# Kernel optimization log

Measured on AMD Instinct MI355X. Metric: run time of the kernel, lower is better.

Reference implementation:

```python
import jax, jax.numpy as jnp
import numpy as np

V_TH = 1.0  # spikingjelly IFNode default threshold; v starts at 0, hard reset after fire


def setup_inputs() -> dict:
    key = jax.random.key(0)
    k_x, k_w1, k_w2 = jax.random.split(key, 3)
    B, IN, FEAT, OUT = 4096, 3136, 6272, 500
    # binary input spikes (LatencyEncoder emits 0/1 spikes per timestep)
    x = (jax.random.uniform(k_x, (B, IN)) < 0.5).astype(jnp.float32)
    # Linear weights, torch layout [out_features, in_features], kaiming-ish scale
    W1 = jax.random.normal(k_w1, (FEAT, IN), dtype=jnp.float32) / np.sqrt(IN)
    W2 = jax.random.normal(k_w2, (OUT, FEAT), dtype=jnp.float32) / np.sqrt(FEAT)
    return {"x": x, "W1": W1, "W2": W2}


def reference(x, W1, W2):
    # Linear (no bias) -> IF neuron single step: v = 0 + I; spike = (v >= V_TH); hard reset
    v1 = x @ W1.T                      # [B, FEAT]
    s1 = (v1 >= V_TH).astype(x.dtype)  # binary hidden spikes
    v2 = s1 @ W2.T                     # [B, OUT]
    s2 = (v2 >= V_TH).astype(x.dtype)  # output spikes
    return s2
```

## Files before the change

kernel.cpp:

```cpp
#include <hip/hip_runtime.h>


namespace {
constexpr int kB = 4096;
constexpr int kIn = 3136;
constexpr int kFeat = 6272;
constexpr int kFeatWords = 196;
constexpr int kOut = 500;
constexpr size_t kPlane1 = (size_t)kFeat * kIn;
constexpr size_t kW1F = 3 * kPlane1;
constexpr size_t kW2F = (size_t)784 * 12288;
constexpr size_t kS1Bytes = (size_t)kB * kFeatWords * 4;
constexpr size_t kXb2Bytes = (size_t)49 * kB * 8;
constexpr unsigned kCap1 = 2u << 20;
constexpr unsigned kCap2 = 1u << 16;
__device__ constexpr double kTau1 = 7.4769e-4;
__device__ constexpr double kTau2 = 1.4955e-3;
}

typedef int v4i __attribute__((ext_vector_type(4)));
typedef int v16i __attribute__((ext_vector_type(16)));

__device__ __forceinline__ void gload_lds16(const void* g, void* l) {
  __builtin_amdgcn_global_load_lds((__attribute__((address_space(1))) void*)(g),
                                   (__attribute__((address_space(3))) void*)(l),
                                   16, 0, 0);
}

__device__ __forceinline__ v4i expand16(unsigned b) {
  unsigned u0 = (((b      ) & 0xFu) * 0x204081u) & 0x01010101u;
  unsigned u1 = (((b >> 4 ) & 0xFu) * 0x204081u) & 0x01010101u;
  unsigned u2 = (((b >> 8 ) & 0xFu) * 0x204081u) & 0x01010101u;
  unsigned u3 = (((b >> 12) & 0xFu) * 0x204081u) & 0x01010101u;
  return (v4i){(int)u0, (int)u1, (int)u2, (int)u3};
}

__device__ __forceinline__ void split3(float w, signed char* d) {
  float c = rintf(w * 128.f);
  d[0] = (signed char)(int)c;
  float r = fmaf(c, -7.8125e-03f, w);
  c = rintf(r * 16384.f);
  d[1] = (signed char)(int)c;
  r = fmaf(c, -6.103515625e-05f, r);
  c = rintf(r * 2097152.f);
  d[2] = (signed char)(int)c;
}

__global__ __launch_bounds__(256) void conv_w1F(const float* __restrict__ W,
                                                signed char* __restrict__ F) {
  const int bx = blockIdx.x;
  const int fb = bx / 49;
  const int kt = bx % 49;
  const int f = threadIdx.x & 63;
  const int g = threadIdx.x >> 6;
  const float* src = W + (size_t)(fb * 64 + f) * kIn + kt * 64 + g * 16;
  union { signed char c[16]; int4 v; } o[3];
#pragma unroll
  for (int q = 0; q < 4; ++q) {
    const float4 w = *(const float4*)(src + q * 4);
    signed char d[4][3];
    split3(w.x, d[0]); split3(w.y, d[1]); split3(w.z, d[2]); split3(w.w, d[3]);
#pragma unroll
    for (int e = 0; e < 4; ++e)
#pragma unroll
      for (int j = 0; j < 3; ++j) o[j].c[q * 4 + e] = d[e][j];
  }
#pragma unroll
  for (int j = 0; j < 3; ++j)
    *(int4*)(F + ((size_t)bx * 3 + j) * 4096 + g * 1024 + f * 16) = o[j].v;
}

__global__ __launch_bounds__(256) void conv_w2F(const float* __restrict__ W,
                                                signed char* __restrict__ F) {
  const int bx = blockIdx.x;
  const int fb = bx / 98;
  const int kt = bx % 98;
  const int f = threadIdx.x & 63;
  const int g = threadIdx.x >> 6;
  const int feat = fb * 64 + f;
  union { signed char c[16]; int4 v; } o[3];
#pragma unroll
  for (int q = 0; q < 4; ++q) {
    float4 w = {0.f, 0.f, 0.f, 0.f};
    if (feat < kOut)
      w = *(const float4*)(W + (size_t)feat * kFeat + kt * 64 + g * 16 + q * 4);
    signed char d[4][3];
    split3(w.x, d[0]); split3(w.y, d[1]); split3(w.z, d[2]); split3(w.w, d[3]);
#pragma unroll
    for (int e = 0; e < 4; ++e)
#pragma unroll
      for (int j = 0; j < 3; ++j) o[j].c[q * 4 + e] = d[e][j];
  }
#pragma unroll
  for (int j = 0; j < 3; ++j)
    *(int4*)(F + ((size_t)bx * 3 + j) * 4096 + g * 1024 + f * 16) = o[j].v;
}

__global__ __launch_bounds__(256) void pack_x2(const float* __restrict__ X,
                                               uint2* __restrict__ xb2) {
  const int wid = (blockIdx.x * 256 + threadIdx.x) >> 6;
  const int lane = threadIdx.x & 63;
  const int b = wid / 49;
  const int g = wid % 49;
  const float v = X[(size_t)b * kIn + g * 64 + lane];
  const unsigned long long bal = __ballot(v != 0.f);
  if (lane == 0) xb2[(size_t)g * kB + b] = make_uint2((unsigned)bal, (unsigned)(bal >> 32));
}

__global__ __launch_bounds__(512, 4) void fc1_v10(
    const uint2* __restrict__ xb2, const signed char* __restrict__ w1lF,
    unsigned* __restrict__ s1b, unsigned* __restrict__ s1T,
    unsigned* __restrict__ cnt, unsigned* __restrict__ list) {
  __shared__ __align__(16) signed char lds[24576];
  const int tid = threadIdx.x;
  const int lane = tid & 63;
  const int ln31 = lane & 31;
  const int half = lane >> 5;
  const int wv = tid >> 6;
  const int waveM = wv >> 1;
  const int waveN = wv & 1;

  const int lin = blockIdx.x + 16 * blockIdx.y;
  const int sw = (lin & 7) * 196 + (lin >> 3);
  const int bx = sw >> 4;
  const int bM = (sw & 15) * 256;

  const signed char* const gbase = w1lF + (size_t)bx * 49 * 12288;
  const bool has1 = (wv < 4);
  const unsigned sG0 = wv * 1024u + lane * 16u;
  const unsigned sL0 = wv * 1024u;
  const unsigned sG1 = (wv + 8) * 1024u + lane * 16u;
  const unsigned sL1 = (wv + 8) * 1024u;

  const uint2* const aptr = xb2 + bM + waveM * 64 + ln31;
  const unsigned bfeat = (waveN * 32 + ln31) * 16u;

  v16i acc[2][3] = {};
  uint2 aC0, aC1, aN0, aN1;

  gload_lds16(gbase + sG0, lds + sL0);
  if (has1) gload_lds16(gbase + sG1, lds + sL1);
  aC0 = aptr[0];
  aC1 = aptr[32];
  const uint2* apn = aptr + (size_t)kB;
  const signed char* gstage = gbase + 12288;

  for (int kt = 0; kt < 49; ++kt) {
    __syncthreads();
    const int cb = (kt & 1) * 12288;
    if (kt < 48) {
      const int nb = ((kt + 1) & 1) * 12288;
      gload_lds16(gstage + sG0, lds + nb + sL0);
      if (has1) gload_lds16(gstage + sG1, lds + nb + sL1);
      gstage += 12288;
      aN0 = apn[0];
      aN1 = apn[32];
      apn += (size_t)kB;
    }
#pragma unroll
    for (int kk = 0; kk < 2; ++kk) {
      const unsigned gsel = (kk * 2 + half) * 1024u;
      const v4i b0 = *(const v4i*)(lds + cb + 0 * 4096 + gsel + bfeat);
      const v4i b1 = *(const v4i*)(lds + cb + 1 * 4096 + gsel + bfeat);
      const v4i b2 = *(const v4i*)(lds + cb + 2 * 4096 + gsel + bfeat);
      const unsigned w0 = kk ? aC0.y : aC0.x;
      const v4i a0 = expand16((w0 >> (half * 16)) & 0xFFFFu);
      acc[0][0] = __builtin_amdgcn_mfma_i32_32x32x32_i8(a0, b0, acc[0][0], 0, 0, 0);
      acc[0][1] = __builtin_amdgcn_mfma_i32_32x32x32_i8(a0, b1, acc[0][1], 0, 0, 0);
      acc[0][2] = __builtin_amdgcn_mfma_i32_32x32x32_i8(a0, b2, acc[0][2], 0, 0, 0);
      const unsigned w1 = kk ? aC1.y : aC1.x;
      const v4i a1 = expand16((w1 >> (half * 16)) & 0xFFFFu);
      acc[1][0] = __builtin_amdgcn_mfma_i32_32x32x32_i8(a1, b0, acc[1][0], 0, 0, 0);
      acc[1][1] = __builtin_amdgcn_mfma_i32_32x32x32_i8(a1, b1, acc[1][1], 0, 0, 0);
      acc[1][2] = __builtin_amdgcn_mfma_i32_32x32x32_i8(a1, b2, acc[1][2], 0, 0, 0);
    }
    aC0 = aN0;
    aC1 = aN1;
  }

  const double s7 = 0.0078125;
  const int word = bx * 2 + waveN;
  const int fcol = word * 32 + ln31;
#pragma unroll
  for (int sub = 0; sub < 2; ++sub) {
#pragma unroll
    for (int t = 0; t < 16; ++t) {
      double v = (double)acc[sub][2][t];
      v = v * s7 + (double)acc[sub][1][t];
      v = v * s7 + (double)acc[sub][0][t];
      v = v * s7;
      const unsigned long long bal = __ballot(v >= 1.0);
      const int mrow = bM + waveM * 64 + sub * 32 + (t & 3) + 8 * (t >> 2);
      if (lane == 0) {
        s1b[(size_t)mrow * kFeatWords + word] = (unsigned)bal;
        s1T[(size_t)word * kB + mrow] = (unsigned)bal;
      }
      if (lane == 32) {
        s1b[(size_t)(mrow + 4) * kFeatWords + word] = (unsigned)(bal >> 32);
        s1T[(size_t)word * kB + mrow + 4] = (unsigned)(bal >> 32);
      }
      if (fabs(v - 1.0) <= kTau1) {
        const unsigned idx = atomicAdd(cnt, 1u);
        if (idx < kCap1) list[idx] = ((unsigned)(mrow + 4 * half) << 13) | (unsigned)fcol;
      }
    }
  }
}

__global__ __launch_bounds__(256) void fc1_correct(
    const float* __restrict__ x, const float* __restrict__ W1,
    const unsigned* __restrict__ cnt, const unsigned* __restrict__ list,
    unsigned* __restrict__ s1b, unsigned* __restrict__ s1T) {
  const unsigned n = min(cnt[0], kCap1);
  const int lane = threadIdx.x & 63;
  const int wid = (blockIdx.x * 256 + threadIdx.x) >> 6;
  const int nw = (gridDim.x * 256) >> 6;
  for (unsigned i = wid; i < n; i += nw) {
    const unsigned u = list[i];
    const int b = (int)(u >> 13);
    const int f = (int)(u & 8191u);
    double s = 0.0;
    for (int k = lane; k < kIn; k += 64)
      s = fma((double)x[(size_t)b * kIn + k], (double)W1[(size_t)f * kIn + k], s);
#pragma unroll
    for (int off = 32; off > 0; off >>= 1) s += __shfl_down(s, off);
    if (lane == 0) {
      const unsigned mask = 1u << (f & 31);
      unsigned* p1 = s1b + (size_t)b * kFeatWords + (f >> 5);
      unsigned* p2 = s1T + (size_t)(f >> 5) * kB + b;
      if (s >= 1.0) { atomicOr(p1, mask); atomicOr(p2, mask); }
      else          { atomicAnd(p1, ~mask); atomicAnd(p2, ~mask); }
    }
  }
}

__global__ __launch_bounds__(128, 4) void fc2_v7(
    const unsigned* __restrict__ s1T, const signed char* __restrict__ w2lF,
    float* __restrict__ out, unsigned* __restrict__ cnt,
    unsigned* __restrict__ list) {
  const int tid = threadIdx.x;
  const int lane = tid & 63;
  const int ln31 = lane & 31;
  const int half = lane >> 5;
  const int wvN = tid >> 6;

  const int lin = blockIdx.x + 128 * blockIdx.y;
  const int sw = ((lin & 7) << 7) + (lin >> 3);
  const int bx = sw >> 7;
  const int bM = (sw & 127) * 32;

  const unsigned* const aptr = s1T + bM + ln31;
  const int fl = wvN * 32 + ln31;
  const signed char* const bbase =
      w2lF + (size_t)(bx * 98) * 12288 + half * 1024u + fl * 16u;

  v16i acc[3] = {};
  v4i b0[6], b1[6];
  uint2 a0, a1;

#define LOAD_TILE(nk, bf, ab)                                   \
  {                                                             \
    const signed char* bp = bbase + (size_t)(nk) * 12288;       \
    bf[0] = *(const v4i*)(bp);                                  \
    bf[1] = *(const v4i*)(bp + 2048);                           \
    bf[2] = *(const v4i*)(bp + 4096);                           \
    bf[3] = *(const v4i*)(bp + 6144);                           \
    bf[4] = *(const v4i*)(bp + 8192);                           \
    bf[5] = *(const v4i*)(bp + 10240);                          \
    (ab).x = aptr[(size_t)((nk) * 2) * kB];                     \
    (ab).y = aptr[(size_t)((nk) * 2 + 1) * kB];                 \
  }
#define COMPUTE_TILE(bf, ab)                                                    \
  {                                                                             \
    _Pragma("unroll")                                                           \
    for (int kk = 0; kk < 2; ++kk) {                                            \
      const unsigned word = kk ? (ab).y : (ab).x;                               \
      const v4i a = expand16((word >> (half * 16)) & 0xFFFFu);                  \
      acc[0] = __builtin_amdgcn_mfma_i32_32x32x32_i8(a, bf[kk], acc[0], 0,0,0); \
      acc[1] = __builtin_amdgcn_mfma_i32_32x32x32_i8(a, bf[2+kk], acc[1],0,0,0);\
      acc[2] = __builtin_amdgcn_mfma_i32_32x32x32_i8(a, bf[4+kk], acc[2],0,0,0);\
    }                                                                           \
  }

  LOAD_TILE(0, b0, a0);
  for (int kt = 0; kt + 2 <= 98; kt += 2) {
    LOAD_TILE(kt + 1, b1, a1);
    COMPUTE_TILE(b0, a0);
    const int nk2 = (kt + 2 < 98) ? kt + 2 : 97;
    LOAD_TILE(nk2, b0, a0);
    COMPUTE_TILE(b1, a1);
  }

  const double s7 = 0.0078125;
  const int o = bx * 64 + wvN * 32 + ln31;
#pragma unroll
  for (int t = 0; t < 16; ++t) {
    double v = (double)acc[2][t];
    v = v * s7 + (double)acc[1][t];
    v = v * s7 + (double)acc[0][t];
    v = v * s7;
    const int b = bM + (t & 3) + 8 * (t >> 2) + 4 * half;
    if (o < kOut) {
      out[(size_t)b * kOut + o] = (v >= 1.0) ? 1.0f : 0.0f;
      if (fabs(v - 1.0) <= kTau2) {
        const unsigned idx = atomicAdd(cnt, 1u);
        if (idx < kCap2) list[idx] = ((unsigned)b << 13) | (unsigned)o;
      }
    }
  }
#undef LOAD_TILE
#undef COMPUTE_TILE
}

__global__ __launch_bounds__(256) void fc2_correct(
    const unsigned* __restrict__ s1b, const float* __restrict__ W2,
    const unsigned* __restrict__ cnt, const unsigned* __restrict__ list,
    float* __restrict__ out) {
  const unsigned n = min(cnt[0], kCap2);
  const int lane = threadIdx.x & 63;
  const int wid = (blockIdx.x * 256 + threadIdx.x) >> 6;
  const int nw = (gridDim.x * 256) >> 6;
  for (unsigned i = wid; i < n; i += nw) {
    const unsigned u = list[i];
    const int b = (int)(u >> 13);
    const int o = (int)(u & 8191u);
    double s = 0.0;
    for (int k = lane; k < kFeat; k += 64) {
      const unsigned w = s1b[(size_t)b * kFeatWords + (k >> 5)];
      if ((w >> (k & 31)) & 1u) s += (double)W2[(size_t)o * kFeat + k];
    }
#pragma unroll
    for (int off = 32; off > 0; off >>= 1) s += __shfl_down(s, off);
    if (lane == 0) out[(size_t)b * kOut + o] = (s >= 1.0) ? 1.0f : 0.0f;
  }
}

__global__ __launch_bounds__(256) void snn_fc1(const float* __restrict__ x,
                                               const float* __restrict__ W1,
                                               unsigned int* __restrict__ s1bits) {
  __shared__ double Xd[32][66];
  __shared__ double Wd[32][66];
  __shared__ unsigned int spikes[64][2];
  const int tid = threadIdx.x;
  const int tx = tid & 15;
  const int ty = tid >> 4;
  const int b0 = blockIdx.y * 64;
  const int f0 = blockIdx.x * 64;
  if (tid < 128) spikes[tid >> 1][tid & 1] = 0u;
  double acc[4][4];
#pragma unroll
  for (int j = 0; j < 4; ++j)
#pragma unroll
    for (int i = 0; i < 4; ++i) acc[j][i] = 0.0;
  const int rl = tid >> 2;
  const int kq = (tid & 3) * 8;
  const float* xrow = x + (size_t)(b0 + rl) * kIn + kq;
  const float* wrow = W1 + (size_t)(f0 + rl) * kIn + kq;
  for (int kc = 0; kc < kIn; kc += 32) {
    const float4 xv0 = *(const float4*)(xrow + kc);
    const float4 xv1 = *(const float4*)(xrow + kc + 4);
    const float4 wv0 = *(const float4*)(wrow + kc);
    const float4 wv1 = *(const float4*)(wrow + kc + 4);
    __syncthreads();
    Xd[kq + 0][rl] = (double)xv0.x; Xd[kq + 1][rl] = (double)xv0.y;
    Xd[kq + 2][rl] = (double)xv0.z; Xd[kq + 3][rl] = (double)xv0.w;
    Xd[kq + 4][rl] = (double)xv1.x; Xd[kq + 5][rl] = (double)xv1.y;
    Xd[kq + 6][rl] = (double)xv1.z; Xd[kq + 7][rl] = (double)xv1.w;
    Wd[kq + 0][rl] = (double)wv0.x; Wd[kq + 1][rl] = (double)wv0.y;
    Wd[kq + 2][rl] = (double)wv0.z; Wd[kq + 3][rl] = (double)wv0.w;
    Wd[kq + 4][rl] = (double)wv1.x; Wd[kq + 5][rl] = (double)wv1.y;
    Wd[kq + 6][rl] = (double)wv1.z; Wd[kq + 7][rl] = (double)wv1.w;
    __syncthreads();
#pragma unroll
    for (int k = 0; k < 32; ++k) {
      const double2 xa = *(const double2*)&Xd[k][ty * 4];
      const double2 xb = *(const double2*)&Xd[k][ty * 4 + 2];
      const double2 wa = *(const double2*)&Wd[k][tx * 4];
      const double2 wb = *(const double2*)&Wd[k][tx * 4 + 2];
      const double xv[4] = {xa.x, xa.y, xb.x, xb.y};
      const double wv[4] = {wa.x, wa.y, wb.x, wb.y};
#pragma unroll
      for (int j = 0; j < 4; ++j)
#pragma unroll
        for (int i = 0; i < 4; ++i) acc[j][i] += xv[j] * wv[i];
    }
  }
  __syncthreads();
#pragma unroll
  for (int j = 0; j < 4; ++j) {
    unsigned int nib = 0u;
#pragma unroll
    for (int i = 0; i < 4; ++i) nib |= (acc[j][i] >= 1.0 ? 1u : 0u) << i;
    atomicOr(&spikes[ty * 4 + j][tx >> 3], nib << ((tx * 4) & 31));
  }
  __syncthreads();
  if (tid < 128) {
    const int r = tid >> 1;
    const int w = tid & 1;
    s1bits[(size_t)(b0 + r) * kFeatWords + (f0 >> 5) + w] = spikes[r][w];
  }
}

__global__ __launch_bounds__(256) void snn_fc2(const unsigned int* __restrict__ s1bits,
                                               const float* __restrict__ W2,
                                               float* __restrict__ out) {
  __shared__ double Wd[32][66];
  __shared__ unsigned int Sb[64];
  const int tid = threadIdx.x;
  const int tx = tid & 15;
  const int ty = tid >> 4;
  const int b0 = blockIdx.y * 64;
  const int o0 = blockIdx.x * 64;
  double acc[4][4];
#pragma unroll
  for (int j = 0; j < 4; ++j)
#pragma unroll
    for (int i = 0; i < 4; ++i) acc[j][i] = 0.0;
  const int rl = tid >> 2;
  const int kq = (tid & 3) * 8;
  int orow = o0 + rl;
  if (orow >= kOut) orow = kOut - 1;
  const float* wrow = W2 + (size_t)orow * kFeat + kq;
  for (int kc = 0; kc < kFeat; kc += 32) {
    const float4 wv0 = *(const float4*)(wrow + kc);
    const float4 wv1 = *(const float4*)(wrow + kc + 4);
    unsigned int sword = 0u;
    if (tid < 64) sword = s1bits[(size_t)(b0 + tid) * kFeatWords + (kc >> 5)];
    __syncthreads();
    Wd[kq + 0][rl] = (double)wv0.x; Wd[kq + 1][rl] = (double)wv0.y;
    Wd[kq + 2][rl] = (double)wv0.z; Wd[kq + 3][rl] = (double)wv0.w;
    Wd[kq + 4][rl] = (double)wv1.x; Wd[kq + 5][rl] = (double)wv1.y;
    Wd[kq + 6][rl] = (double)wv1.z; Wd[kq + 7][rl] = (double)wv1.w;
    if (tid < 64) Sb[tid] = sword;
    __syncthreads();
    const unsigned int rw0 = Sb[ty * 4 + 0];
    const unsigned int rw1 = Sb[ty * 4 + 1];
    const unsigned int rw2 = Sb[ty * 4 + 2];
    const unsigned int rw3 = Sb[ty * 4 + 3];
#pragma unroll
    for (int k = 0; k < 32; ++k) {
      const double2 wa = *(const double2*)&Wd[k][tx * 4];
      const double2 wb = *(const double2*)&Wd[k][tx * 4 + 2];
      const double wv[4] = {wa.x, wa.y, wb.x, wb.y};
      const double sv[4] = {(double)((rw0 >> k) & 1u), (double)((rw1 >> k) & 1u),
                            (double)((rw2 >> k) & 1u), (double)((rw3 >> k) & 1u)};
#pragma unroll
      for (int j = 0; j < 4; ++j)
#pragma unroll
        for (int i = 0; i < 4; ++i) acc[j][i] += sv[j] * wv[i];
    }
  }
#pragma unroll
  for (int j = 0; j < 4; ++j) {
    const int b = b0 + ty * 4 + j;
#pragma unroll
    for (int i = 0; i < 4; ++i) {
      const int o = o0 + tx * 4 + i;
      if (o < kOut) out[(size_t)b * kOut + o] = (acc[j][i] >= 1.0) ? 1.0f : 0.0f;
    }
  }
}

extern "C" void kernel_launch(void* const* d_in, const int* in_sizes, int n_in,
                              void* d_out, int out_size, void* d_ws, size_t ws_size,
                              hipStream_t stream) {
  const float* x = (const float*)d_in[0];
  const float* W1 = (const float*)d_in[1];
  const float* W2 = (const float*)d_in[2];
  float* out = (float*)d_out;

  char* p = (char*)d_ws;
  signed char* w1lF = (signed char*)p;   p += kW1F;
  signed char* w2lF = (signed char*)p;   p += kW2F;
  unsigned* s1b = (unsigned*)p;          p += kS1Bytes;
  unsigned* s1T = (unsigned*)p;          p += kS1Bytes;
  uint2* xb2 = (uint2*)p;                p += kXb2Bytes;
  unsigned* list1 = (unsigned*)p;        p += (size_t)kCap1 * 4;
  unsigned* list2 = (unsigned*)p;        p += (size_t)kCap2 * 4;
  unsigned* ctrs = (unsigned*)p;         p += 256;
  const size_t need = (size_t)(p - (char*)d_ws);

  if (ws_size >= need) {
    hipMemsetAsync(ctrs, 0, 32, stream);
    conv_w1F<<<4802, 256, 0, stream>>>(W1, w1lF);
    conv_w2F<<<784, 256, 0, stream>>>(W2, w2lF);
    pack_x2<<<50176, 256, 0, stream>>>(x, xb2);
    fc1_v10<<<dim3(16, 98), 512, 0, stream>>>(xb2, w1lF, s1b, s1T, ctrs, list1);
    fc1_correct<<<1024, 256, 0, stream>>>(x, W1, ctrs, list1, s1b, s1T);
    fc2_v7<<<dim3(128, 8), 128, 0, stream>>>(s1T, w2lF, out, ctrs + 4, list2);
    fc2_correct<<<64, 256, 0, stream>>>(s1b, W2, ctrs + 4, list2, out);
  } else {
    unsigned* s1 = (unsigned*)d_ws;
    snn_fc1<<<dim3(98, 64), 256, 0, stream>>>(x, W1, s1);
    snn_fc2<<<dim3(8, 64), 256, 0, stream>>>(s1, W2, out);
  }
}
```

Before: 576.3 us.

## Pre-expand input spikes to int8 MFMA-ready layout instead of bitpacked words

Replaces the bit-packed input format with an int8 layout pre-tiled to match the MFMA A-operand fragment order. The fc1 kernel can then load A fragments directly with 16-byte loads instead of expanding bits in registers each iteration. The pack kernel becomes fewer, wider blocks doing coalesced float4 reads. In exchange, fc1 reads 8x more A-operand bytes from global memory and more registers are live; launch bounds drop to 2 blocks per SM and the correction-list capacity is halved.

```diff
diff --git a/kernel.cpp b/kernel.cpp
--- a/kernel.cpp
+++ b/kernel.cpp
@@ -11,8 +11,8 @@
 constexpr size_t kW1F = 3 * kPlane1;
 constexpr size_t kW2F = (size_t)784 * 12288;
 constexpr size_t kS1Bytes = (size_t)kB * kFeatWords * 4;
-constexpr size_t kXb2Bytes = (size_t)49 * kB * 8;
-constexpr unsigned kCap1 = 2u << 20;
+constexpr size_t kX8Bytes = (size_t)49 * 256 * 1024;
+constexpr unsigned kCap1 = 1u << 20;
 constexpr unsigned kCap2 = 1u << 16;
 __device__ constexpr double kTau1 = 7.4769e-4;
 __device__ constexpr double kTau2 = 1.4955e-3;
@@ -96,19 +96,30 @@
     *(int4*)(F + ((size_t)bx * 3 + j) * 4096 + g * 1024 + f * 16) = o[j].v;
 }
 
-__global__ __launch_bounds__(256) void pack_x2(const float* __restrict__ X,
-                                               uint2* __restrict__ xb2) {
-  const int wid = (blockIdx.x * 256 + threadIdx.x) >> 6;
+__global__ __launch_bounds__(256) void pack_x8(const float* __restrict__ X,
+                                               signed char* __restrict__ xb8) {
+  const int slot = blockIdx.x * 4 + (threadIdx.x >> 6);
   const int lane = threadIdx.x & 63;
-  const int b = wid / 49;
-  const int g = wid % 49;
-  const float v = X[(size_t)b * kIn + g * 64 + lane];
-  const unsigned long long bal = __ballot(v != 0.f);
-  if (lane == 0) xb2[(size_t)g * kB + b] = make_uint2((unsigned)bal, (unsigned)(bal >> 32));
-}
-
-__global__ __launch_bounds__(512, 4) void fc1_v10(
-    const uint2* __restrict__ xb2, const signed char* __restrict__ w1lF,
+  const int kk = slot & 1;
+  const int mgrp = (slot >> 1) & 127;
+  const int kt = slot >> 8;
+  const int row = mgrp * 32 + (lane & 31);
+  const int k0 = kt * 64 + kk * 32 + (lane >> 5) * 16;
+  const float* src = X + (size_t)row * kIn + k0;
+  union { signed char c[16]; int4 v; } o;
+#pragma unroll
+  for (int q = 0; q < 4; ++q) {
+    const float4 w = *(const float4*)(src + q * 4);
+    o.c[q * 4 + 0] = (w.x != 0.f) ? 1 : 0;
+    o.c[q * 4 + 1] = (w.y != 0.f) ? 1 : 0;
+    o.c[q * 4 + 2] = (w.z != 0.f) ? 1 : 0;
+    o.c[q * 4 + 3] = (w.w != 0.f) ? 1 : 0;
+  }
+  *(int4*)(xb8 + (size_t)slot * 1024 + lane * 16) = o.v;
+}
+
+__global__ __launch_bounds__(512, 2) void fc1_v11(
+    const signed char* __restrict__ xb8, const signed char* __restrict__ w1lF,
     unsigned* __restrict__ s1b, unsigned* __restrict__ s1T,
     unsigned* __restrict__ cnt, unsigned* __restrict__ list) {
   __shared__ __align__(16) signed char lds[24576];
@@ -132,17 +143,22 @@
   const unsigned sG1 = (wv + 8) * 1024u + lane * 16u;
   const unsigned sL1 = (wv + 8) * 1024u;
 
-  const uint2* const aptr = xb2 + bM + waveM * 64 + ln31;
+  const int gmgrp0 = (bM >> 5) + waveM * 2;
+  const signed char* apn =
+      xb8 + ((size_t)gmgrp0 * 2) * 1024 + lane * 16u;
   const unsigned bfeat = (waveN * 32 + ln31) * 16u;
 
   v16i acc[2][3] = {};
-  uint2 aC0, aC1, aN0, aN1;
+  v4i c00, c01, c10, c11;
+  v4i n00, n01, n10, n11;
 
   gload_lds16(gbase + sG0, lds + sL0);
   if (has1) gload_lds16(gbase + sG1, lds + sL1);
-  aC0 = aptr[0];
-  aC1 = aptr[32];
-  const uint2* apn = aptr + (size_t)kB;
+  c00 = *(const v4i*)(apn);
+  c01 = *(const v4i*)(apn + 1024);
+  c10 = *(const v4i*)(apn + 2048);
+  c11 = *(const v4i*)(apn + 3072);
+  apn += 262144;
   const signed char* gstage = gbase + 12288;
 
   for (int kt = 0; kt < 49; ++kt) {
@@ -153,29 +169,37 @@
       gload_lds16(gstage + sG0, lds + nb + sL0);
       if (has1) gload_lds16(gstage + sG1, lds + nb + sL1);
       gstage += 12288;
-      aN0 = apn[0];
-      aN1 = apn[32];
-      apn += (size_t)kB;
-    }
-#pragma unroll
-    for (int kk = 0; kk < 2; ++kk) {
-      const unsigned gsel = (kk * 2 + half) * 1024u;
+      n00 = *(const v4i*)(apn);
+      n01 = *(const v4i*)(apn + 1024);
+      n10 = *(const v4i*)(apn + 2048);
+      n11 = *(const v4i*)(apn + 3072);
+      apn += 262144;
+    }
+    {
+      const unsigned gsel = half * 1024u;
       const v4i b0 = *(const v4i*)(lds + cb + 0 * 4096 + gsel + bfeat);
       const v4i b1 = *(const v4i*)(lds + cb + 1 * 4096 + gsel + bfeat);
       const v4i b2 = *(const v4i*)(lds + cb + 2 * 4096 + gsel + bfeat);
-      const unsigned w0 = kk ? aC0.y : aC0.x;
-      const v4i a0 = expand16((w0 >> (half * 16)) & 0xFFFFu);
-      acc[0][0] = __builtin_amdgcn_mfma_i32_32x32x32_i8(a0, b0, acc[0][0], 0, 0, 0);
-      acc[0][1] = __builtin_amdgcn_mfma_i32_32x32x32_i8(a0, b1, acc[0][1], 0, 0, 0);
-      acc[0][2] = __builtin_amdgcn_mfma_i32_32x32x32_i8(a0, b2, acc[0][2], 0, 0, 0);
-      const unsigned w1 = kk ? aC1.y : aC1.x;
-      const v4i a1 = expand16((w1 >> (half * 16)) & 0xFFFFu);
-      acc[1][0] = __builtin_amdgcn_mfma_i32_32x32x32_i8(a1, b0, acc[1][0], 0, 0, 0);
-      acc[1][1] = __builtin_amdgcn_mfma_i32_32x32x32_i8(a1, b1, acc[1][1], 0, 0, 0);
-      acc[1][2] = __builtin_amdgcn_mfma_i32_32x32x32_i8(a1, b2, acc[1][2], 0, 0, 0);
-    }
-    aC0 = aN0;
-    aC1 = aN1;
+      acc[0][0] = __builtin_amdgcn_mfma_i32_32x32x32_i8(c00, b0, acc[0][0], 0, 0, 0);
+      acc[0][1] = __builtin_amdgcn_mfma_i32_32x32x32_i8(c00, b1, acc[0][1], 0, 0, 0);
+      acc[0][2] = __builtin_amdgcn_mfma_i32_32x32x32_i8(c00, b2, acc[0][2], 0, 0, 0);
+      acc[1][0] = __builtin_amdgcn_mfma_i32_32x32x32_i8(c10, b0, acc[1][0], 0, 0, 0);
+      acc[1][1] = __builtin_amdgcn_mfma_i32_32x32x32_i8(c10, b1, acc[1][1], 0, 0, 0);
+      acc[1][2] = __builtin_amdgcn_mfma_i32_32x32x32_i8(c10, b2, acc[1][2], 0, 0, 0);
+    }
+    {
+      const unsigned gsel = (2 + half) * 1024u;
+      const v4i b0 = *(const v4i*)(lds + cb + 0 * 4096 + gsel + bfeat);
+      const v4i b1 = *(const v4i*)(lds + cb + 1 * 4096 + gsel + bfeat);
+      const v4i b2 = *(const v4i*)(lds + cb + 2 * 4096 + gsel + bfeat);
+      acc[0][0] = __builtin_amdgcn_mfma_i32_32x32x32_i8(c01, b0, acc[0][0], 0, 0, 0);
+      acc[0][1] = __builtin_amdgcn_mfma_i32_32x32x32_i8(c01, b1, acc[0][1], 0, 0, 0);
+      acc[0][2] = __builtin_amdgcn_mfma_i32_32x32x32_i8(c01, b2, acc[0][2], 0, 0, 0);
+      acc[1][0] = __builtin_amdgcn_mfma_i32_32x32x32_i8(c11, b0, acc[1][0], 0, 0, 0);
+      acc[1][1] = __builtin_amdgcn_mfma_i32_32x32x32_i8(c11, b1, acc[1][1], 0, 0, 0);
+      acc[1][2] = __builtin_amdgcn_mfma_i32_32x32x32_i8(c11, b2, acc[1][2], 0, 0, 0);
+    }
+    c00 = n00; c01 = n01; c10 = n10; c11 = n11;
   }
 
   const double s7 = 0.0078125;
@@ -474,7 +498,7 @@
   signed char* w2lF = (signed char*)p;   p += kW2F;
   unsigned* s1b = (unsigned*)p;          p += kS1Bytes;
   unsigned* s1T = (unsigned*)p;          p += kS1Bytes;
-  uint2* xb2 = (uint2*)p;                p += kXb2Bytes;
+  signed char* xb8 = (signed char*)p;    p += kX8Bytes;
   unsigned* list1 = (unsigned*)p;        p += (size_t)kCap1 * 4;
   unsigned* list2 = (unsigned*)p;        p += (size_t)kCap2 * 4;
   unsigned* ctrs = (unsigned*)p;         p += 256;
@@ -484,8 +508,8 @@
     hipMemsetAsync(ctrs, 0, 32, stream);
     conv_w1F<<<4802, 256, 0, stream>>>(W1, w1lF);
     conv_w2F<<<784, 256, 0, stream>>>(W2, w2lF);
-    pack_x2<<<50176, 256, 0, stream>>>(x, xb2);
-    fc1_v10<<<dim3(16, 98), 512, 0, stream>>>(xb2, w1lF, s1b, s1T, ctrs, list1);
+    pack_x8<<<3136, 256, 0, stream>>>(x, xb8);
+    fc1_v11<<<dim3(16, 98), 512, 0, stream>>>(xb8, w1lF, s1b, s1T, ctrs, list1);
     fc1_correct<<<1024, 256, 0, stream>>>(x, W1, ctrs, list1, s1b, s1T);
     fc2_v7<<<dim3(128, 8), 128, 0, stream>>>(s1T, w2lF, out, ctrs + 4, list2);
     fc2_correct<<<64, 256, 0, stream>>>(s1b, W2, ctrs + 4, list2, out);
```

Measured after the change: 681.1 us. +18.2%, slower.

## Triple-buffer fc1 LDS pipeline with split-phase barriers and MFMA priority

Applied to the files above, without the earlier changes.

Replaces the double-buffered fc1 main loop with a three-stage LDS ring (prefetch two tiles ahead), split into two half-K phases, each with explicit vmcnt/lgkmcnt waits, barriers, sched_barrier and s_setprio around the MFMA block. The aim is to hide global-to-LDS load latency and keep the matrix cores busy. In exchange, LDS use per block grows, the occupancy hint drops from 4 to 2, and each tile now has more barriers. The list1 capacity is also halved.

```diff
diff --git a/kernel.cpp b/kernel.cpp
--- a/kernel.cpp
+++ b/kernel.cpp
@@ -12,7 +12,7 @@
 constexpr size_t kW2F = (size_t)784 * 12288;
 constexpr size_t kS1Bytes = (size_t)kB * kFeatWords * 4;
 constexpr size_t kXb2Bytes = (size_t)49 * kB * 8;
-constexpr unsigned kCap1 = 2u << 20;
+constexpr unsigned kCap1 = 1u << 20;
 constexpr unsigned kCap2 = 1u << 16;
 __device__ constexpr double kTau1 = 7.4769e-4;
 __device__ constexpr double kTau2 = 1.4955e-3;
@@ -107,11 +107,11 @@
   if (lane == 0) xb2[(size_t)g * kB + b] = make_uint2((unsigned)bal, (unsigned)(bal >> 32));
 }
 
-__global__ __launch_bounds__(512, 4) void fc1_v10(
+__global__ __launch_bounds__(512, 2) void fc1_v12(
     const uint2* __restrict__ xb2, const signed char* __restrict__ w1lF,
     unsigned* __restrict__ s1b, unsigned* __restrict__ s1T,
     unsigned* __restrict__ cnt, unsigned* __restrict__ list) {
-  __shared__ __align__(16) signed char lds[24576];
+  __shared__ __align__(16) signed char lds[36864];
   const int tid = threadIdx.x;
   const int lane = tid & 63;
   const int ln31 = lane & 31;
@@ -137,46 +137,89 @@
 
   v16i acc[2][3] = {};
   uint2 aC0, aC1, aN0, aN1;
-
+  v4i a00, a10, a01, a11;
+
+  aC0 = aptr[0];
+  aC1 = aptr[32];
   gload_lds16(gbase + sG0, lds + sL0);
   if (has1) gload_lds16(gbase + sG1, lds + sL1);
-  aC0 = aptr[0];
-  aC1 = aptr[32];
+  gload_lds16(gbase + 12288 + sG0, lds + 12288 + sL0);
+  if (has1) gload_lds16(gbase + 12288 + sG1, lds + 12288 + sL1);
+  if (has1) asm volatile("s_waitcnt vmcnt(2)" ::: "memory");
+  else      asm volatile("s_waitcnt vmcnt(1)" ::: "memory");
+  __builtin_amdgcn_s_barrier();
+  asm volatile("" ::: "memory");
+
   const uint2* apn = aptr + (size_t)kB;
-  const signed char* gstage = gbase + 12288;
-
-  for (int kt = 0; kt < 49; ++kt) {
-    __syncthreads();
-    const int cb = (kt & 1) * 12288;
-    if (kt < 48) {
-      const int nb = ((kt + 1) & 1) * 12288;
-      gload_lds16(gstage + sG0, lds + nb + sL0);
-      if (has1) gload_lds16(gstage + sG1, lds + nb + sL1);
-      gstage += 12288;
-      aN0 = apn[0];
-      aN1 = apn[32];
-      apn += (size_t)kB;
-    }
-#pragma unroll
-    for (int kk = 0; kk < 2; ++kk) {
-      const unsigned gsel = (kk * 2 + half) * 1024u;
-      const v4i b0 = *(const v4i*)(lds + cb + 0 * 4096 + gsel + bfeat);
-      const v4i b1 = *(const v4i*)(lds + cb + 1 * 4096 + gsel + bfeat);
-      const v4i b2 = *(const v4i*)(lds + cb + 2 * 4096 + gsel + bfeat);
-      const unsigned w0 = kk ? aC0.y : aC0.x;
-      const v4i a0 = expand16((w0 >> (half * 16)) & 0xFFFFu);
-      acc[0][0] = __builtin_amdgcn_mfma_i32_32x32x32_i8(a0, b0, acc[0][0], 0, 0, 0);
-      acc[0][1] = __builtin_amdgcn_mfma_i32_32x32x32_i8(a0, b1, acc[0][1], 0, 0, 0);
-      acc[0][2] = __builtin_amdgcn_mfma_i32_32x32x32_i8(a0, b2, acc[0][2], 0, 0, 0);
-      const unsigned w1 = kk ? aC1.y : aC1.x;
-      const v4i a1 = expand16((w1 >> (half * 16)) & 0xFFFFu);
-      acc[1][0] = __builtin_amdgcn_mfma_i32_32x32x32_i8(a1, b0, acc[1][0], 0, 0, 0);
-      acc[1][1] = __builtin_amdgcn_mfma_i32_32x32x32_i8(a1, b1, acc[1][1], 0, 0, 0);
-      acc[1][2] = __builtin_amdgcn_mfma_i32_32x32x32_i8(a1, b2, acc[1][2], 0, 0, 0);
-    }
-    aC0 = aN0;
-    aC1 = aN1;
-  }
+  const signed char* gst = gbase + 2 * 12288;
+
+#define FC1_MM(AS0, AS1, B0, B1, B2)                                          \
+  acc[0][0] = __builtin_amdgcn_mfma_i32_32x32x32_i8(AS0, B0, acc[0][0],0,0,0);\
+  acc[0][1] = __builtin_amdgcn_mfma_i32_32x32x32_i8(AS0, B1, acc[0][1],0,0,0);\
+  acc[0][2] = __builtin_amdgcn_mfma_i32_32x32x32_i8(AS0, B2, acc[0][2],0,0,0);\
+  acc[1][0] = __builtin_amdgcn_mfma_i32_32x32x32_i8(AS1, B0, acc[1][0],0,0,0);\
+  acc[1][1] = __builtin_amdgcn_mfma_i32_32x32x32_i8(AS1, B1, acc[1][1],0,0,0);\
+  acc[1][2] = __builtin_amdgcn_mfma_i32_32x32x32_i8(AS1, B2, acc[1][2],0,0,0)
+
+#define FC1_PH0(CB, SB, DO_A, DO_S)                                           \
+  {                                                                           \
+    a00 = expand16((aC0.x >> (half * 16)) & 0xFFFFu);                         \
+    a10 = expand16((aC1.x >> (half * 16)) & 0xFFFFu);                         \
+    a01 = expand16((aC0.y >> (half * 16)) & 0xFFFFu);                         \
+    a11 = expand16((aC1.y >> (half * 16)) & 0xFFFFu);                         \
+    const v4i b0 = *(const v4i*)(lds + (CB) + 0 * 4096 + half * 1024u + bfeat);\
+    const v4i b1 = *(const v4i*)(lds + (CB) + 1 * 4096 + half * 1024u + bfeat);\
+    const v4i b2 = *(const v4i*)(lds + (CB) + 2 * 4096 + half * 1024u + bfeat);\
+    if (DO_A) { aN0 = apn[0]; aN1 = apn[32]; apn += (size_t)kB; }             \
+    if (DO_S) { gload_lds16(gst + sG0, lds + (SB) + sL0); }                   \
+    asm volatile("" ::: "memory");                                            \
+    __builtin_amdgcn_s_barrier();                                             \
+    asm volatile("s_waitcnt lgkmcnt(0)" ::: "memory");                        \
+    __builtin_amdgcn_sched_barrier(0);                                        \
+    __builtin_amdgcn_s_setprio(1);                                            \
+    FC1_MM(a00, a10, b0, b1, b2);                                             \
+    __builtin_amdgcn_s_setprio(0);                                            \
+    __builtin_amdgcn_s_barrier();                                             \
+    asm volatile("" ::: "memory");                                            \
+  }
+
+#define FC1_PH1(CB, SB, DO_S, WAITM)                                          \
+  {                                                                           \
+    const v4i b0 = *(const v4i*)(lds + (CB) + 0 * 4096 + (2 + half) * 1024u + bfeat);\
+    const v4i b1 = *(const v4i*)(lds + (CB) + 1 * 4096 + (2 + half) * 1024u + bfeat);\
+    const v4i b2 = *(const v4i*)(lds + (CB) + 2 * 4096 + (2 + half) * 1024u + bfeat);\
+    if ((DO_S) && has1) { gload_lds16(gst + sG1, lds + (SB) + sL1); }         \
+    if ((DO_S)) gst += 12288;                                                 \
+    if ((WAITM) == 2) {                                                       \
+      if (has1) asm volatile("s_waitcnt vmcnt(2)" ::: "memory");              \
+      else      asm volatile("s_waitcnt vmcnt(1)" ::: "memory");              \
+    } else if ((WAITM) == 0) {                                                \
+      asm volatile("s_waitcnt vmcnt(0)" ::: "memory");                        \
+    }                                                                         \
+    asm volatile("" ::: "memory");                                            \
+    __builtin_amdgcn_s_barrier();                                             \
+    asm volatile("s_waitcnt lgkmcnt(0)" ::: "memory");                        \
+    __builtin_amdgcn_sched_barrier(0);                                        \
+    __builtin_amdgcn_s_setprio(1);                                            \
+    FC1_MM(a01, a11, b0, b1, b2);                                             \
+    __builtin_amdgcn_s_setprio(0);                                            \
+    __builtin_amdgcn_s_barrier();                                             \
+    asm volatile("" ::: "memory");                                            \
+    aC0 = aN0; aC1 = aN1;                                                     \
+  }
+
+  for (int t = 0; t < 15; ++t) {
+    FC1_PH0(0,     24576, 1, 1); FC1_PH1(0,     24576, 1, 2);
+    FC1_PH0(12288, 0,     1, 1); FC1_PH1(12288, 0,     1, 2);
+    FC1_PH0(24576, 12288, 1, 1); FC1_PH1(24576, 12288, 1, 2);
+  }
+  FC1_PH0(0,     24576, 1, 1); FC1_PH1(0,     24576, 1, 2);
+  FC1_PH0(12288, 0,     1, 1); FC1_PH1(12288, 0,     1, 2);
+  FC1_PH0(24576, 0,     1, 0); FC1_PH1(24576, 0,     0, 0);
+  FC1_PH0(0,     0,     0, 0); FC1_PH1(0,     0,     0, -1);
+#undef FC1_PH0
+#undef FC1_PH1
+#undef FC1_MM
 
   const double s7 = 0.0078125;
   const int word = bx * 2 + waveN;
@@ -485,7 +528,7 @@
     conv_w1F<<<4802, 256, 0, stream>>>(W1, w1lF);
     conv_w2F<<<784, 256, 0, stream>>>(W2, w2lF);
     pack_x2<<<50176, 256, 0, stream>>>(x, xb2);
-    fc1_v10<<<dim3(16, 98), 512, 0, stream>>>(xb2, w1lF, s1b, s1T, ctrs, list1);
+    fc1_v12<<<dim3(16, 98), 512, 0, stream>>>(xb2, w1lF, s1b, s1T, ctrs, list1);
     fc1_correct<<<1024, 256, 0, stream>>>(x, W1, ctrs, list1, s1b, s1T);
     fc2_v7<<<dim3(128, 8), 128, 0, stream>>>(s1T, w2lF, out, ctrs + 4, list2);
     fc2_correct<<<64, 256, 0, stream>>>(s1b, W2, ctrs + 4, list2, out);
```

Measured after the change: 662.4 us. 1.15x slower.

## Replace LDS-staged fc1 GEMM with register-prefetched direct global loads

Applied to the files above, without the earlier changes.

The fc1 int8 MFMA kernel drops LDS staging and block-wide barriers. Each 2-wave block now covers a 128x64 tile, loads B fragments straight from global memory into registers, and software-pipelines the next half-step's loads behind the current MFMAs. Each wave now does four M sub-tiles instead of two, so more accumulator registers are live per wave. The correction list capacity is halved. This removes __syncthreads and LDS traffic at the cost of more global/L2 reads of W1 (no sharing across waves in a block), higher register pressure, and a smaller overflow margin for the correction list.

```diff
diff --git a/kernel.cpp b/kernel.cpp
--- a/kernel.cpp
+++ b/kernel.cpp
@@ -12,7 +12,7 @@
 constexpr size_t kW2F = (size_t)784 * 12288;
 constexpr size_t kS1Bytes = (size_t)kB * kFeatWords * 4;
 constexpr size_t kXb2Bytes = (size_t)49 * kB * 8;
-constexpr unsigned kCap1 = 2u << 20;
+constexpr unsigned kCap1 = 1u << 20;
 constexpr unsigned kCap2 = 1u << 16;
 __device__ constexpr double kTau1 = 7.4769e-4;
 __device__ constexpr double kTau2 = 1.4955e-3;
@@ -20,12 +20,6 @@
 
 typedef int v4i __attribute__((ext_vector_type(4)));
 typedef int v16i __attribute__((ext_vector_type(16)));
-
-__device__ __forceinline__ void gload_lds16(const void* g, void* l) {
-  __builtin_amdgcn_global_load_lds((__attribute__((address_space(1))) void*)(g),
-                                   (__attribute__((address_space(3))) void*)(l),
-                                   16, 0, 0);
-}
 
 __device__ __forceinline__ v4i expand16(unsigned b) {
   unsigned u0 = (((b      ) & 0xFu) * 0x204081u) & 0x01010101u;
@@ -107,82 +101,76 @@
   if (lane == 0) xb2[(size_t)g * kB + b] = make_uint2((unsigned)bal, (unsigned)(bal >> 32));
 }
 
-__global__ __launch_bounds__(512, 4) void fc1_v10(
+__global__ __launch_bounds__(128, 2) void fc1_v13(
     const uint2* __restrict__ xb2, const signed char* __restrict__ w1lF,
     unsigned* __restrict__ s1b, unsigned* __restrict__ s1T,
     unsigned* __restrict__ cnt, unsigned* __restrict__ list) {
-  __shared__ __align__(16) signed char lds[24576];
   const int tid = threadIdx.x;
   const int lane = tid & 63;
   const int ln31 = lane & 31;
   const int half = lane >> 5;
-  const int wv = tid >> 6;
-  const int waveM = wv >> 1;
-  const int waveN = wv & 1;
-
-  const int lin = blockIdx.x + 16 * blockIdx.y;
-  const int sw = (lin & 7) * 196 + (lin >> 3);
-  const int bx = sw >> 4;
-  const int bM = (sw & 15) * 256;
-
-  const signed char* const gbase = w1lF + (size_t)bx * 49 * 12288;
-  const bool has1 = (wv < 4);
-  const unsigned sG0 = wv * 1024u + lane * 16u;
-  const unsigned sL0 = wv * 1024u;
-  const unsigned sG1 = (wv + 8) * 1024u + lane * 16u;
-  const unsigned sL1 = (wv + 8) * 1024u;
-
-  const uint2* const aptr = xb2 + bM + waveM * 64 + ln31;
-  const unsigned bfeat = (waveN * 32 + ln31) * 16u;
-
-  v16i acc[2][3] = {};
-  uint2 aC0, aC1, aN0, aN1;
-
-  gload_lds16(gbase + sG0, lds + sL0);
-  if (has1) gload_lds16(gbase + sG1, lds + sL1);
-  aC0 = aptr[0];
-  aC1 = aptr[32];
-  const uint2* apn = aptr + (size_t)kB;
-  const signed char* gstage = gbase + 12288;
+  const int wvN = tid >> 6;
+
+  const int lin = blockIdx.x + 32 * blockIdx.y;
+  const int sw = (lin & 7) * 392 + (lin >> 3);
+  const int bx = sw >> 5;
+  const int bM = (sw & 31) * 128;
+
+  const signed char* const gb = w1lF + (size_t)bx * 49 * 12288;
+  const unsigned hsel = half * 1024u + (wvN * 32 + ln31) * 16u;
+  const uint2* const aptr = xb2 + bM + ln31;
+
+  v16i acc[4][3] = {};
+  v4i b0[3], b1[3];
+  uint2 aC[4], aN[4];
+
+#define FC1_LB(KT, KK, BF)                                                    \
+  {                                                                           \
+    const signed char* bp_ = gb + (size_t)(KT) * 12288 + (KK) * 2048 + hsel;  \
+    (BF)[0] = *(const v4i*)(bp_);                                             \
+    (BF)[1] = *(const v4i*)(bp_ + 4096);                                      \
+    (BF)[2] = *(const v4i*)(bp_ + 8192);                                      \
+  }
+#define FC1_LA(KT, AR)                                                        \
+  {                                                                           \
+    _Pragma("unroll")                                                         \
+    for (int s = 0; s < 4; ++s) (AR)[s] = aptr[(size_t)(KT) * kB + s * 32];   \
+  }
+#define FC1_COMP(BF, AW, SEL)                                                 \
+  {                                                                           \
+    _Pragma("unroll")                                                         \
+    for (int s = 0; s < 4; ++s) {                                             \
+      const unsigned w_ = (SEL) ? (AW)[s].y : (AW)[s].x;                      \
+      const v4i a_ = expand16((w_ >> (half * 16)) & 0xFFFFu);                 \
+      acc[s][0] = __builtin_amdgcn_mfma_i32_32x32x32_i8(a_, (BF)[0], acc[s][0], 0, 0, 0); \
+      acc[s][1] = __builtin_amdgcn_mfma_i32_32x32x32_i8(a_, (BF)[1], acc[s][1], 0, 0, 0); \
+      acc[s][2] = __builtin_amdgcn_mfma_i32_32x32x32_i8(a_, (BF)[2], acc[s][2], 0, 0, 0); \
+    }                                                                         \
+  }
+
+  FC1_LB(0, 0, b0);
+  FC1_LA(0, aC);
+#pragma unroll
+  for (int s = 0; s < 4; ++s) aN[s] = aC[s];
 
   for (int kt = 0; kt < 49; ++kt) {
-    __syncthreads();
-    const int cb = (kt & 1) * 12288;
-    if (kt < 48) {
-      const int nb = ((kt + 1) & 1) * 12288;
-      gload_lds16(gstage + sG0, lds + nb + sL0);
-      if (has1) gload_lds16(gstage + sG1, lds + nb + sL1);
-      gstage += 12288;
-      aN0 = apn[0];
-      aN1 = apn[32];
-      apn += (size_t)kB;
-    }
-#pragma unroll
-    for (int kk = 0; kk < 2; ++kk) {
-      const unsigned gsel = (kk * 2 + half) * 1024u;
-      const v4i b0 = *(const v4i*)(lds + cb + 0 * 4096 + gsel + bfeat);
-      const v4i b1 = *(const v4i*)(lds + cb + 1 * 4096 + gsel + bfeat);
-      const v4i b2 = *(const v4i*)(lds + cb + 2 * 4096 + gsel + bfeat);
-      const unsigned w0 = kk ? aC0.y : aC0.x;
-      const v4i a0 = expand16((w0 >> (half * 16)) & 0xFFFFu);
-      acc[0][0] = __builtin_amdgcn_mfma_i32_32x32x32_i8(a0, b0, acc[0][0], 0, 0, 0);
-      acc[0][1] = __builtin_amdgcn_mfma_i32_32x32x32_i8(a0, b1, acc[0][1], 0, 0, 0);
-      acc[0][2] = __builtin_amdgcn_mfma_i32_32x32x32_i8(a0, b2, acc[0][2], 0, 0, 0);
-      const unsigned w1 = kk ? aC1.y : aC1.x;
-      const v4i a1 = expand16((w1 >> (half * 16)) & 0xFFFFu);
-      acc[1][0] = __builtin_amdgcn_mfma_i32_32x32x32_i8(a1, b0, acc[1][0], 0, 0, 0);
-      acc[1][1] = __builtin_amdgcn_mfma_i32_32x32x32_i8(a1, b1, acc[1][1], 0, 0, 0);
-      acc[1][2] = __builtin_amdgcn_mfma_i32_32x32x32_i8(a1, b2, acc[1][2], 0, 0, 0);
-    }
-    aC0 = aN0;
-    aC1 = aN1;
-  }
+    FC1_LB(kt, 1, b1);
+    if (kt < 48) FC1_LA(kt + 1, aN);
+    FC1_COMP(b0, aC, 0);
+    if (kt < 48) FC1_LB(kt + 1, 0, b0);
+    FC1_COMP(b1, aC, 1);
+#pragma unroll
+    for (int s = 0; s < 4; ++s) aC[s] = aN[s];
+  }
+#undef FC1_LB
+#undef FC1_LA
+#undef FC1_COMP
 
   const double s7 = 0.0078125;
-  const int word = bx * 2 + waveN;
+  const int word = bx * 2 + wvN;
   const int fcol = word * 32 + ln31;
 #pragma unroll
-  for (int sub = 0; sub < 2; ++sub) {
+  for (int sub = 0; sub < 4; ++sub) {
 #pragma unroll
     for (int t = 0; t < 16; ++t) {
       double v = (double)acc[sub][2][t];
@@ -190,7 +178,7 @@
       v = v * s7 + (double)acc[sub][0][t];
       v = v * s7;
       const unsigned long long bal = __ballot(v >= 1.0);
-      const int mrow = bM + waveM * 64 + sub * 32 + (t & 3) + 8 * (t >> 2);
+      const int mrow = bM + sub * 32 + (t & 3) + 8 * (t >> 2);
       if (lane == 0) {
         s1b[(size_t)mrow * kFeatWords + word] = (unsigned)bal;
         s1T[(size_t)word * kB + mrow] = (unsigned)bal;
@@ -485,7 +473,7 @@
     conv_w1F<<<4802, 256, 0, stream>>>(W1, w1lF);
     conv_w2F<<<784, 256, 0, stream>>>(W2, w2lF);
     pack_x2<<<50176, 256, 0, stream>>>(x, xb2);
-    fc1_v10<<<dim3(16, 98), 512, 0, stream>>>(xb2, w1lF, s1b, s1T, ctrs, list1);
+    fc1_v13<<<dim3(32, 98), 128, 0, stream>>>(xb2, w1lF, s1b, s1T, ctrs, list1);
     fc1_correct<<<1024, 256, 0, stream>>>(x, W1, ctrs, list1, s1b, s1T);
     fc2_v7<<<dim3(128, 8), 128, 0, stream>>>(s1T, w2lF, out, ctrs + 4, list2);
     fc2_correct<<<64, 256, 0, stream>>>(s1b, W2, ctrs + 4, list2, out);
```

Measured after the change: 564.9 us. -2.0%, faster.
